# Kernel tuning notes

Measured on AMD Instinct MI355X. Metric: run time of the kernel, lower is better.

Reference implementation:

```python
import jax, jax.numpy as jnp
import numpy as np

B, M, IN_DIM, D, H, NL = 4, 2048, 512, 1024, 4, 2
HD = D // H           # head_dim = 256
HD2 = HD // 2
ROPE_BASE = 10000.0
LN_EPS = 1e-5


def setup_inputs() -> dict:
    key = jax.random.key(0)
    ks = jax.random.split(key, 9)
    s = 0.02
    return {
        "x": jax.random.normal(ks[0], (B, M, IN_DIM), jnp.float32),
        "positions": jnp.sort(jax.random.randint(ks[1], (B, M), 0, 8192), axis=-1).astype(jnp.int32),
        "mask": jnp.ones((B, M), jnp.float32),
        "in_w": jax.random.normal(ks[2], (IN_DIM, D), jnp.float32) * s,
        "in_b": jnp.zeros((D,), jnp.float32),
        "qkv_w": jax.random.normal(ks[3], (NL, D, 3 * D), jnp.float32) * s,
        "o_w": jax.random.normal(ks[4], (NL, D, D), jnp.float32) * s,
        "ln1_g": jnp.ones((NL, D), jnp.float32),
        "ln1_b": jnp.zeros((NL, D), jnp.float32),
        "ffn_w1": jax.random.normal(ks[5], (NL, D, 4 * D), jnp.float32) * s,
        "ffn_b1": jnp.zeros((NL, 4 * D), jnp.float32),
        "ffn_w2": jax.random.normal(ks[6], (NL, 4 * D, D), jnp.float32) * s,
        "ffn_b2": jnp.zeros((NL, D), jnp.float32),
        "ln2_g": jnp.ones((NL, D), jnp.float32),
        "ln2_b": jnp.zeros((NL, D), jnp.float32),
        "start_state": jax.random.normal(ks[7], (D,), jnp.float32) * 0.02,
    }


def _layernorm(x, g, b):
    mu = jnp.mean(x, axis=-1, keepdims=True)
    var = jnp.mean((x - mu) ** 2, axis=-1, keepdims=True)
    return (x - mu) * jax.lax.rsqrt(var + LN_EPS) * g + b


def _rope_cos_sin(positions):
    # rope_module(pos): angles over head_dim//2 freqs, shared across heads
    inv_freq = 1.0 / (ROPE_BASE ** (jnp.arange(HD2, dtype=jnp.float32) * 2.0 / HD))
    ang = positions.astype(jnp.float32)[:, :, None] * inv_freq  # (B, L, HD2)
    return jnp.cos(ang), jnp.sin(ang)


def _apply_rotary(x, cos, sin):
    # x: (B, H, L, HD); cos/sin: (B, 1, L, HD2) broadcast over heads
    x1, x2 = x[..., :HD2], x[..., HD2:]
    return jnp.concatenate([x1 * cos - x2 * sin, x1 * sin + x2 * cos], axis=-1)


def _self_attention(x, cos, sin, mask, qkv_w, o_w):
    Bx, L, Dx = x.shape
    qkv = (x @ qkv_w).reshape(Bx, L, 3, H, HD)
    q = jnp.transpose(qkv[:, :, 0], (0, 2, 1, 3))  # (B, H, L, HD)
    k = jnp.transpose(qkv[:, :, 1], (0, 2, 1, 3))
    v = jnp.transpose(qkv[:, :, 2], (0, 2, 1, 3))
    q = _apply_rotary(q, cos, sin)
    k = _apply_rotary(k, cos, sin)
    scores = jnp.einsum("bhqd,bhkd->bhqk", q, k) * (1.0 / np.sqrt(HD))
    scores = jnp.where(mask[:, None, None, :] == 0, -jnp.inf, scores)
    attn = jax.nn.softmax(scores, axis=-1)
    out = jnp.einsum("bhqk,bhkd->bhqd", attn, v)
    out = jnp.transpose(out, (0, 2, 1, 3)).reshape(Bx, L, Dx)
    return out @ o_w


def reference(x, positions, mask, in_w, in_b, qkv_w, o_w, ln1_g, ln1_b,
              ffn_w1, ffn_b1, ffn_w2, ffn_b2, ln2_g, ln2_b, start_state):
    h = x @ in_w + in_b  # (B, M, D)
    cos, sin = _rope_cos_sin(positions)
    cos, sin = cos[:, None], sin[:, None]  # (B, 1, M, HD2)
    for l in range(NL):
        h = h + _self_attention(_layernorm(h, ln1_g[l], ln1_b[l]), cos, sin, mask,
                                qkv_w[l], o_w[l])
        y = _layernorm(h, ln2_g[l], ln2_b[l])
        y = jax.nn.gelu(y @ ffn_w1[l] + ffn_b1[l], approximate=False) @ ffn_w2[l] + ffn_b2[l]
        h = h + y
    lengths = jnp.sum(mask, axis=1)
    last_idx = jnp.clip(lengths.astype(jnp.int32) - 1, 0, None)
    gathered = h[jnp.arange(h.shape[0]), last_idx]  # (B, D)
    has_hist = lengths > 0
    return jnp.where(has_hist[:, None], gathered, start_state[None, :])
```

## Files before the change

kernel.cpp:

```cpp
#include <hip/hip_runtime.h>
#include <math.h>

typedef __attribute__((ext_vector_type(8))) short bf16x8;
typedef __attribute__((ext_vector_type(4))) float floatx4;
typedef __attribute__((ext_vector_type(4))) unsigned short ushort4v;

typedef __attribute__((address_space(1))) void as1_void;
typedef __attribute__((address_space(3))) void as3_void;

static __device__ __forceinline__ unsigned short f2b(float f) {
    union { float f; unsigned u; } v; v.f = f;
    unsigned r = v.u + 0x7fffu + ((v.u >> 16) & 1u);
    return (unsigned short)(r >> 16);
}
static __device__ __forceinline__ float b2f(unsigned short h) {
    union { unsigned u; float f; } v; v.u = ((unsigned)h) << 16;
    return v.f;
}

template<int P> __device__ __forceinline__ void waitcnt_vm() {
    if constexpr (P == 0)      asm volatile("s_waitcnt vmcnt(0)" ::: "memory");
    else if constexpr (P == 2) asm volatile("s_waitcnt vmcnt(2)" ::: "memory");
    else if constexpr (P == 3) asm volatile("s_waitcnt vmcnt(3)" ::: "memory");
    else if constexpr (P == 4) asm volatile("s_waitcnt vmcnt(4)" ::: "memory");
    else if constexpr (P == 6) asm volatile("s_waitcnt vmcnt(6)" ::: "memory");
    else                       asm volatile("s_waitcnt vmcnt(8)" ::: "memory");
}

template<int TM, int TN>
__global__ __launch_bounds__(512, 2) void gemm9(
    const unsigned short* __restrict__ A,
    const unsigned short* __restrict__ Bt,
    float* __restrict__ Cf, unsigned short* __restrict__ Cb,
    const float* __restrict__ bias,
    int K, int lda, int ldb, int ldc,
    int zdiv, long a_s1, long a_s2, long b_s1, long b_s2, long c_s1, long c_s2,
    int mode)
{
    constexpr int FM  = TM / 32;
    constexpr int FN  = TN / 64;
    constexpr int MH  = (FM == 8) ? 2 : 1;
    constexpr int NH  = (FN == 4) ? 2 : 1;
    constexpr int NPH = MH * NH;
    constexpr int FMp = FM / MH;
    constexpr int FNp = FN / NH;
    constexpr int NRA = TM / 64;
    constexpr int NRB = TN / 64;

    __shared__ unsigned short As[2][8 * TM * 8];
    __shared__ unsigned short Bs[2][8 * TN * 8];

    const int tid  = threadIdx.x;
    const int wid  = tid >> 6;
    const int lane = tid & 63;
    const int q    = lane >> 4;
    const int r    = lane & 15;
    const int wm   = wid >> 2;
    const int wn   = wid & 3;

    const int z  = blockIdx.z;
    const int zq = z / zdiv, zr = z % zdiv;
    const long offC = (long)zq * c_s1 + (long)zr * c_s2;

    const int m0 = blockIdx.y * TM;
    const int n0 = blockIdx.x * TN;

    const unsigned short* Ab = A  + (long)zq * a_s1 + (long)zr * a_s2 + (long)m0 * lda;
    const unsigned short* Bb = Bt + (long)zq * b_s1 + (long)zr * b_s2 + (long)n0 * ldb;

    floatx4 acc[FM][FN];
    #pragma unroll
    for (int i = 0; i < FM; ++i)
        #pragma unroll
        for (int j = 0; j < FN; ++j)
            acc[i][j] = (floatx4){0.f, 0.f, 0.f, 0.f};

    const int nk = K >> 6;

    auto stageA = [&](int kt, int slot) {
        const int kofs = (kt << 6) + (wid << 3);
        #pragma unroll
        for (int rb = 0; rb < NRA; ++rb)
            __builtin_amdgcn_global_load_lds(
                (as1_void*)(void*)(Ab + (long)(rb * 64 + lane) * lda + kofs),
                (as3_void*)&As[slot][(wid * TM + rb * 64) * 8], 16, 0, 0);
    };
    auto stageB = [&](int kt, int slot) {
        const int kofs = (kt << 6) + (wid << 3);
        #pragma unroll
        for (int rb = 0; rb < NRB; ++rb)
            __builtin_amdgcn_global_load_lds(
                (as1_void*)(void*)(Bb + (long)(rb * 64 + lane) * ldb + kofs),
                (as3_void*)&Bs[slot][(wid * TN + rb * 64) * 8], 16, 0, 0);
    };

    stageA(0, 0);
    stageB(0, 0);
    waitcnt_vm<0>();
    asm volatile("s_barrier" ::: "memory");

    for (int kt = 0; kt < nk; ++kt) {
        const int c  = kt & 1;
        const int sl = c ^ 1;
        const bool pf = (kt + 1 < nk);

        bf16x8 af[MH][FMp][2];
        bf16x8 bf_[NH][FNp][2];

        #pragma unroll
        for (int ph = 0; ph < NPH; ++ph) {
            const int mh = (MH == 1) ? 0 : ((NPH == 4) ? (ph >> 1) : ph);
            const int nh = (NH == 1) ? 0 : ((NPH == 4) ? (((ph + 1) >> 1) & 1) : ph);
            const bool readA = (ph == mh * (NPH / MH));
            const bool readB = (ph == nh);

            if (readA) {
                #pragma unroll
                for (int i = 0; i < FMp; ++i)
                    #pragma unroll
                    for (int ks = 0; ks < 2; ++ks)
                        af[mh][i][ks] = *(const bf16x8*)&As[c][
                            ((ks * 4 + q) * TM + wm * (TM / 2) + mh * (FMp * 16) + i * 16 + r) * 8];
            }
            if (readB) {
                #pragma unroll
                for (int j = 0; j < FNp; ++j)
                    #pragma unroll
                    for (int ks = 0; ks < 2; ++ks)
                        bf_[nh][j][ks] = *(const bf16x8*)&Bs[c][
                            ((ks * 4 + q) * TN + wn * (TN / 4) + nh * (FNp * 16) + j * 16 + r) * 8];
            }
            if (ph == 0 && pf) stageA(kt + 1, sl);
            if (ph == 1 && pf) stageB(kt + 1, sl);

            asm volatile("s_barrier" ::: "memory");
            asm volatile("s_waitcnt lgkmcnt(0)" ::: "memory");
            __builtin_amdgcn_s_setprio(1);
            #pragma unroll
            for (int i = 0; i < FMp; ++i)
                #pragma unroll
                for (int j = 0; j < FNp; ++j) {
                    acc[mh * FMp + i][nh * FNp + j] = __builtin_amdgcn_mfma_f32_16x16x32_bf16(
                        af[mh][i][0], bf_[nh][j][0], acc[mh * FMp + i][nh * FNp + j], 0, 0, 0);
                    acc[mh * FMp + i][nh * FNp + j] = __builtin_amdgcn_mfma_f32_16x16x32_bf16(
                        af[mh][i][1], bf_[nh][j][1], acc[mh * FMp + i][nh * FNp + j], 0, 0, 0);
                }
            __builtin_amdgcn_s_setprio(0);
        }

        if (pf) {
            waitcnt_vm<0>();
            asm volatile("s_barrier" ::: "memory");
        }
    }

    #pragma unroll
    for (int i = 0; i < FM; ++i) {
        const int gr0 = m0 + wm * (TM / 2) + i * 16 + q * 4;
        #pragma unroll
        for (int j = 0; j < FN; ++j) {
            const int gc = n0 + wn * (TN / 4) + j * 16 + r;
            const float bvl = bias ? bias[gc] : 0.0f;
            #pragma unroll
            for (int rr = 0; rr < 4; ++rr) {
                const long cidx = offC + (long)(gr0 + rr) * ldc + gc;
                float v = acc[i][j][rr] + bvl;
                if (mode == 0) {
                    Cf[cidx] = v;
                } else if (mode == 1) {
                    Cf[cidx] += v;
                } else if (mode == 2) {
                    Cb[cidx] = f2b(v);
                } else {
                    Cb[cidx] = f2b(0.5f * v * (1.0f + erff(v * 0.70710678118654752f)));
                }
            }
        }
    }
}

template<int T>
__global__ __launch_bounds__(256) void gemm_bf16(
    const unsigned short* __restrict__ A,
    const unsigned short* __restrict__ Bt,
    float* __restrict__ Cf, unsigned short* __restrict__ Cb,
    const float* __restrict__ bias,
    int K, int lda, int ldb, int ldc,
    int zdiv, long a_s1, long a_s2, long b_s1, long b_s2, long c_s1, long c_s2,
    int mode)
{
    constexpr int F  = T / 32;
    constexpr int NR = T / 64;

    __shared__ unsigned short As[3][4 * T * 8];
    __shared__ unsigned short Bs[3][4 * T * 8];

    const int tid  = threadIdx.x;
    const int wid  = tid >> 6;
    const int lane = tid & 63;
    const int q    = lane >> 4;
    const int r    = lane & 15;

    const int z  = blockIdx.z;
    const int zq = z / zdiv, zr = z % zdiv;
    const long offC = (long)zq * c_s1 + (long)zr * c_s2;

    const int m0 = blockIdx.y * T;
    const int n0 = blockIdx.x * T;

    const unsigned short* Ab = A  + (long)zq * a_s1 + (long)zr * a_s2 + (long)m0 * lda;
    const unsigned short* Bb = Bt + (long)zq * b_s1 + (long)zr * b_s2 + (long)n0 * ldb;

    const int wr = (wid >> 1) * (T / 2);
    const int wc = (wid & 1)  * (T / 2);

    floatx4 acc[F][F];
    #pragma unroll
    for (int i = 0; i < F; ++i)
        #pragma unroll
        for (int j = 0; j < F; ++j)
            acc[i][j] = (floatx4){0.f, 0.f, 0.f, 0.f};

    const int qc = wid;
    const int nk = K >> 5;

    auto stage = [&](int kt, int buf) {
        const int kofs = (kt << 5) + (qc << 3);
        #pragma unroll
        for (int rb = 0; rb < NR; ++rb)
            __builtin_amdgcn_global_load_lds(
                (as1_void*)(void*)(Ab + (long)(lane + rb * 64) * lda + kofs),
                (as3_void*)&As[buf][(qc * T + rb * 64) * 8], 16, 0, 0);
        #pragma unroll
        for (int rb = 0; rb < NR; ++rb)
            __builtin_amdgcn_global_load_lds(
                (as1_void*)(void*)(Bb + (long)(lane + rb * 64) * ldb + kofs),
                (as3_void*)&Bs[buf][(qc * T + rb * 64) * 8], 16, 0, 0);
    };

    stage(0, 0);
    if (nk > 1) {
        stage(1, 1);
        waitcnt_vm<2 * NR>();
    } else {
        waitcnt_vm<0>();
    }
    asm volatile("s_barrier" ::: "memory");

    int cur = 0;
    for (int kt = 0; kt < nk; ++kt) {
        int s2 = cur + 2; if (s2 >= 3) s2 -= 3;
        if (kt + 2 < nk) stage(kt + 2, s2);

        bf16x8 av[F], bv[F];
        #pragma unroll
        for (int i = 0; i < F; ++i)
            av[i] = *(const bf16x8*)&As[cur][(q * T + wr + i * 16 + r) * 8];
        #pragma unroll
        for (int j = 0; j < F; ++j)
            bv[j] = *(const bf16x8*)&Bs[cur][(q * T + wc + j * 16 + r) * 8];
        #pragma unroll
        for (int i = 0; i < F; ++i)
            #pragma unroll
            for (int j = 0; j < F; ++j)
                acc[i][j] = __builtin_amdgcn_mfma_f32_16x16x32_bf16(av[i], bv[j], acc[i][j], 0, 0, 0);

        if (kt + 2 < nk) {
            asm volatile("s_waitcnt lgkmcnt(0)" ::: "memory");
            waitcnt_vm<2 * NR>();
            asm volatile("s_barrier" ::: "memory");
        } else if (kt + 1 < nk) {
            asm volatile("s_waitcnt lgkmcnt(0)" ::: "memory");
            waitcnt_vm<0>();
            asm volatile("s_barrier" ::: "memory");
        }

        cur = (cur + 1 == 3) ? 0 : cur + 1;
    }

    #pragma unroll
    for (int i = 0; i < F; ++i) {
        const int gr0 = m0 + wr + i * 16 + q * 4;
        #pragma unroll
        for (int j = 0; j < F; ++j) {
            const int gc = n0 + wc + j * 16 + r;
            const float bvl = bias ? bias[gc] : 0.0f;
            #pragma unroll
            for (int rr = 0; rr < 4; ++rr) {
                const long cidx = offC + (long)(gr0 + rr) * ldc + gc;
                float v = acc[i][j][rr] + bvl;
                if (mode == 0) {
                    Cf[cidx] = v;
                } else if (mode == 1) {
                    Cf[cidx] += v;
                } else if (mode == 2) {
                    Cb[cidx] = f2b(v);
                } else {
                    Cb[cidx] = f2b(0.5f * v * (1.0f + erff(v * 0.70710678118654752f)));
                }
            }
        }
    }
}

__global__ void transpose_cast_f32(const float* __restrict__ in, unsigned short* __restrict__ out,
                                   int R, int C)
{
    __shared__ float t[32][33];
    const int c0 = blockIdx.x * 32, r0 = blockIdx.y * 32;
    const int tx = threadIdx.x, ty = threadIdx.y;
    #pragma unroll
    for (int i = 0; i < 4; ++i)
        t[ty + i * 8][tx] = in[(long)(r0 + ty + i * 8) * C + c0 + tx];
    __syncthreads();
    #pragma unroll
    for (int i = 0; i < 4; ++i)
        out[(long)(c0 + ty + i * 8) * R + r0 + tx] = f2b(t[tx][ty + i * 8]);
}

__global__ void transpose_v(const unsigned short* __restrict__ qkv, unsigned short* __restrict__ vT)
{
    __shared__ unsigned short t[32][33];
    const int hh = blockIdx.z;
    const int d0 = blockIdx.x * 32, m0 = blockIdx.y * 32;
    const int tx = threadIdx.x, ty = threadIdx.y;
    const unsigned short* ip = qkv + 2048 + hh * 256;
    unsigned short* op = vT + (long)hh * 524288;
    #pragma unroll
    for (int i = 0; i < 4; ++i)
        t[ty + i * 8][tx] = ip[(long)(m0 + ty + i * 8) * 3072 + d0 + tx];
    __syncthreads();
    #pragma unroll
    for (int i = 0; i < 4; ++i)
        op[(long)(d0 + ty + i * 8) * 2048 + m0 + tx] = t[tx][ty + i * 8];
}

__global__ void cast_f32_bf16(const float* __restrict__ in, unsigned short* __restrict__ out)
{
    const long i = (long)blockIdx.x * 256 + threadIdx.x;
    const float4 v = ((const float4*)in)[i];
    ushort4v o;
    o[0] = f2b(v.x); o[1] = f2b(v.y); o[2] = f2b(v.z); o[3] = f2b(v.w);
    ((ushort4v*)out)[i] = o;
}

__global__ void zero_f32(float* __restrict__ p)
{
    p[blockIdx.x * 256 + threadIdx.x] = 0.0f;
}

__global__ __launch_bounds__(256) void ln_kernel(const float* __restrict__ h,
    const float* __restrict__ g, const float* __restrict__ bta,
    unsigned short* __restrict__ out)
{
    const int tok = blockIdx.x;
    const float4 v = ((const float4*)(h + (long)tok * 1024))[threadIdx.x];
    float s  = v.x + v.y + v.z + v.w;
    float s2 = v.x * v.x + v.y * v.y + v.z * v.z + v.w * v.w;
    #pragma unroll
    for (int off = 32; off > 0; off >>= 1) {
        s  += __shfl_xor(s, off);
        s2 += __shfl_xor(s2, off);
    }
    __shared__ float rs[4], rs2[4];
    const int wid = threadIdx.x >> 6, lane = threadIdx.x & 63;
    if (lane == 0) { rs[wid] = s; rs2[wid] = s2; }
    __syncthreads();
    s  = rs[0] + rs[1] + rs[2] + rs[3];
    s2 = rs2[0] + rs2[1] + rs2[2] + rs2[3];
    const float mu = s * (1.0f / 1024.0f);
    float var = s2 * (1.0f / 1024.0f) - mu * mu;
    var = fmaxf(var, 0.0f);
    const float rsg = 1.0f / sqrtf(var + 1e-5f);
    const float4 gv = ((const float4*)g)[threadIdx.x];
    const float4 bv = ((const float4*)bta)[threadIdx.x];
    ushort4v o;
    o[0] = f2b((v.x - mu) * rsg * gv.x + bv.x);
    o[1] = f2b((v.y - mu) * rsg * gv.y + bv.y);
    o[2] = f2b((v.z - mu) * rsg * gv.z + bv.z);
    o[3] = f2b((v.w - mu) * rsg * gv.w + bv.w);
    *(ushort4v*)&out[(long)tok * 1024 + threadIdx.x * 4] = o;
}

__global__ __launch_bounds__(256) void rope_kernel(unsigned short* __restrict__ qkv,
                                                   const int* __restrict__ pos)
{
    const int tok = blockIdx.x;
    const float p = (float)pos[tok];
    unsigned short* base = qkv + (long)tok * 3072;
    #pragma unroll
    for (int it = 0; it < 2; ++it) {
        const int idx = threadIdx.x + it * 256;
        const int hh = idx >> 7, d = idx & 127;
        const float inv = exp2f((float)d * (-13.287712379549449f / 128.0f));
        const float ang = p * inv;
        const float c = cosf(ang), s = sinf(ang);
        unsigned short* qp = base + hh * 256 + d;
        {
            const float x1 = b2f(qp[0]), x2 = b2f(qp[128]);
            qp[0]   = f2b(x1 * c - x2 * s);
            qp[128] = f2b(x1 * s + x2 * c);
        }
        unsigned short* kp = qp + 1024;
        {
            const float x1 = b2f(kp[0]), x2 = b2f(kp[128]);
            kp[0]   = f2b(x1 * c - x2 * s);
            kp[128] = f2b(x1 * s + x2 * c);
        }
    }
}

__global__ __launch_bounds__(256) void softmax_kernel(unsigned short* __restrict__ sc,
                                                      const float* __restrict__ mrow)
{
    unsigned short* row = sc + (long)blockIdx.x * 2048;
    const int t = threadIdx.x;

    float v[8];
    const ushort4v u0 = *(const ushort4v*)&row[t * 8];
    const ushort4v u1 = *(const ushort4v*)&row[t * 8 + 4];
    #pragma unroll
    for (int i = 0; i < 4; ++i) { v[i] = b2f(u0[i]); v[4 + i] = b2f(u1[i]); }

    float mx = -3.0e38f;
    #pragma unroll
    for (int i = 0; i < 8; ++i) {
        const float m = mrow[t * 8 + i];
        v[i] = (m == 0.0f) ? -3.0e38f : v[i] * 0.0625f;
        mx = fmaxf(mx, v[i]);
    }
    #pragma unroll
    for (int off = 32; off > 0; off >>= 1) mx = fmaxf(mx, __shfl_xor(mx, off));
    __shared__ float rmx[4], rsm[4];
    const int wid = t >> 6, lane = t & 63;
    if (lane == 0) rmx[wid] = mx;
    __syncthreads();
    mx = fmaxf(fmaxf(rmx[0], rmx[1]), fmaxf(rmx[2], rmx[3]));

    float s = 0.0f;
    #pragma unroll
    for (int i = 0; i < 8; ++i) { v[i] = expf(v[i] - mx); s += v[i]; }
    #pragma unroll
    for (int off = 32; off > 0; off >>= 1) s += __shfl_xor(s, off);
    if (lane == 0) rsm[wid] = s;
    __syncthreads();
    s = rsm[0] + rsm[1] + rsm[2] + rsm[3];
    const float invs = (s > 0.0f) ? 1.0f / s : 0.0f;

    ushort4v o0, o1;
    #pragma unroll
    for (int i = 0; i < 4; ++i) { o0[i] = f2b(v[i] * invs); o1[i] = f2b(v[4 + i] * invs); }
    *(ushort4v*)&row[t * 8]     = o0;
    *(ushort4v*)&row[t * 8 + 4] = o1;
}

__global__ __launch_bounds__(256) void gather_kernel(const float* __restrict__ h,
    const float* __restrict__ mask, const float* __restrict__ ss, float* __restrict__ out)
{
    const int b = blockIdx.x;
    const float* mrow = mask + b * 2048;
    const int t = threadIdx.x;
    float s = 0.0f;
    #pragma unroll
    for (int i = 0; i < 8; ++i) s += mrow[t * 8 + i];
    #pragma unroll
    for (int off = 32; off > 0; off >>= 1) s += __shfl_xor(s, off);
    __shared__ float red[4];
    if ((t & 63) == 0) red[t >> 6] = s;
    __syncthreads();
    const float len = red[0] + red[1] + red[2] + red[3];
    const int L = (int)len;
    const int last = (L > 0) ? (L - 1) : 0;
    const bool has = len > 0.0f;
    const float* src = has ? (h + ((long)b * 2048 + last) * 1024) : ss;
    #pragma unroll
    for (int i = 0; i < 4; ++i) {
        const int d = t + i * 256;
        out[b * 1024 + d] = src[d];
    }
}

extern "C" void kernel_launch(void* const* d_in, const int* in_sizes, int n_in,
                              void* d_out, int out_size, void* d_ws, size_t ws_size,
                              hipStream_t stream)
{
    (void)in_sizes; (void)n_in; (void)out_size;
    const float* x      = (const float*)d_in[0];
    const int*   pos    = (const int*)d_in[1];
    const float* mask   = (const float*)d_in[2];
    const float* in_w   = (const float*)d_in[3];
    const float* in_b   = (const float*)d_in[4];
    const float* qkv_w  = (const float*)d_in[5];
    const float* o_w    = (const float*)d_in[6];
    const float* ln1_g  = (const float*)d_in[7];
    const float* ln1_b  = (const float*)d_in[8];
    const float* ffn_w1 = (const float*)d_in[9];
    const float* ffn_b1 = (const float*)d_in[10];
    const float* ffn_w2 = (const float*)d_in[11];
    const float* ffn_b2 = (const float*)d_in[12];
    const float* ln2_g  = (const float*)d_in[13];
    const float* ln2_b  = (const float*)d_in[14];
    const float* sstate = (const float*)d_in[15];
    float* out = (float*)d_out;

    const size_t NEED = 143654912ull;
    if (ws_size < NEED) {
        zero_f32<<<16, 256, 0, stream>>>(out);
        return;
    }
    char* w = (char*)d_ws;
    unsigned short* wt_in  = (unsigned short*)(w);
    unsigned short* wt_qkv = (unsigned short*)(w + 1048576);
    unsigned short* wt_o   = (unsigned short*)(w + 7340032);
    unsigned short* wt_f1  = (unsigned short*)(w + 9437184);
    unsigned short* wt_f2  = (unsigned short*)(w + 17825792);
    float*          hbuf   = (float*)(w + 26214400);
    unsigned short* xn_bf  = (unsigned short*)(w + 59768832);
    unsigned short* ao_bf  = (unsigned short*)(w + 76546048);
    unsigned short* qkv_b  = (unsigned short*)(w + 93323264);
    unsigned short* vT_b   = (unsigned short*)(w + 105906176);
    unsigned short* scmid  = (unsigned short*)(w + 110100480);
    unsigned short* x_bf   = ao_bf;
    unsigned short* mid_bf = (unsigned short*)(w + 76546048);

    const dim3 tb(32, 8);

    transpose_cast_f32<<<dim3(32, 16), tb, 0, stream>>>(in_w, wt_in, 512, 1024);
    cast_f32_bf16<<<4096, 256, 0, stream>>>(x, x_bf);

    gemm9<256, 128><<<dim3(8, 32, 1), 512, 0, stream>>>(x_bf, wt_in, hbuf, nullptr, in_b,
        512, 512, 512, 1024, 1, 0, 0, 0, 0, 0, 0, 0);

    for (int l = 0; l < 2; ++l) {
        transpose_cast_f32<<<dim3(96, 32),  tb, 0, stream>>>(qkv_w  + (long)l * 3145728, wt_qkv, 1024, 3072);
        transpose_cast_f32<<<dim3(32, 32),  tb, 0, stream>>>(o_w    + (long)l * 1048576, wt_o,   1024, 1024);
        transpose_cast_f32<<<dim3(128, 32), tb, 0, stream>>>(ffn_w1 + (long)l * 4194304, wt_f1,  1024, 4096);
        transpose_cast_f32<<<dim3(32, 128), tb, 0, stream>>>(ffn_w2 + (long)l * 4194304, wt_f2,  4096, 1024);

        ln_kernel<<<8192, 256, 0, stream>>>(hbuf, ln1_g + l * 1024, ln1_b + l * 1024, xn_bf);

        for (int b = 0; b < 4; ++b) {
            gemm9<128, 256><<<dim3(12, 16, 1), 512, 0, stream>>>(xn_bf + (long)b * 2097152, wt_qkv,
                nullptr, qkv_b, nullptr, 1024, 1024, 1024, 3072, 1, 0, 0, 0, 0, 0, 0, 2);
            rope_kernel<<<2048, 256, 0, stream>>>(qkv_b, pos + b * 2048);
            transpose_v<<<dim3(8, 64, 4), tb, 0, stream>>>(qkv_b, vT_b);
            gemm9<256, 256><<<dim3(8, 8, 4), 512, 0, stream>>>(qkv_b, qkv_b + 1024,
                nullptr, scmid, nullptr, 256, 3072, 3072, 2048,
                1, 256l, 0, 256l, 0, 4194304l, 0, 2);
            softmax_kernel<<<8192, 256, 0, stream>>>(scmid, mask + b * 2048);
            gemm_bf16<64><<<dim3(4, 32, 4), 256, 0, stream>>>(scmid, vT_b,
                nullptr, ao_bf + (long)b * 2097152, nullptr, 2048, 2048, 2048, 1024,
                1, 4194304l, 0, 524288l, 0, 256l, 0, 2);
        }
        gemm9<256, 128><<<dim3(8, 32, 1), 512, 0, stream>>>(ao_bf, wt_o,
            hbuf, nullptr, nullptr, 1024, 1024, 1024, 1024, 1, 0, 0, 0, 0, 0, 0, 1);

        ln_kernel<<<8192, 256, 0, stream>>>(hbuf, ln2_g + l * 1024, ln2_b + l * 1024, xn_bf);

        gemm9<256, 256><<<dim3(16, 32, 1), 512, 0, stream>>>(xn_bf, wt_f1,
            nullptr, mid_bf, ffn_b1 + l * 4096, 1024, 1024, 1024, 4096, 1, 0, 0, 0, 0, 0, 0, 3);
        gemm9<256, 128><<<dim3(8, 32, 1), 512, 0, stream>>>(mid_bf, wt_f2,
            hbuf, nullptr, ffn_b2 + l * 1024, 4096, 4096, 4096, 1024, 1, 0, 0, 0, 0, 0, 0, 1);
    }

    gather_kernel<<<4, 256, 0, stream>>>(hbuf, mask, sstate, out);
}
```

Measured before the change: 2.161 ms.

## Split GEMM tiles into 128-wide LDS units with finer-grained staged prefetch

Restructures the main bf16 MFMA GEMM so each operand tile is split into 128-row LDS units, each with its own slot (up to four per operand). Loads for the next k-step are issued per unit, interleaved between the quadrant MFMA phases, and use partial vmcnt waits. The aim is to overlap global-to-LDS traffic with compute better than the previous whole-tile double buffer did, which waited for all loads at the end of each k-step. In exchange it adds more barriers per k-step, changes the accumulator-to-output mapping, and adds slot-indexing complexity, with some risk to correctness if the waits or slot reuse are misordered.

```diff
diff --git a/kernel.cpp b/kernel.cpp
--- a/kernel.cpp
+++ b/kernel.cpp
@@ -21,14 +21,12 @@
 template<int P> __device__ __forceinline__ void waitcnt_vm() {
     if constexpr (P == 0)      asm volatile("s_waitcnt vmcnt(0)" ::: "memory");
     else if constexpr (P == 2) asm volatile("s_waitcnt vmcnt(2)" ::: "memory");
-    else if constexpr (P == 3) asm volatile("s_waitcnt vmcnt(3)" ::: "memory");
     else if constexpr (P == 4) asm volatile("s_waitcnt vmcnt(4)" ::: "memory");
-    else if constexpr (P == 6) asm volatile("s_waitcnt vmcnt(6)" ::: "memory");
-    else                       asm volatile("s_waitcnt vmcnt(8)" ::: "memory");
+    else                       asm volatile("s_waitcnt vmcnt(6)" ::: "memory");
 }
 
 template<int TM, int TN>
-__global__ __launch_bounds__(512, 2) void gemm9(
+__global__ __launch_bounds__(512, 2) void gemmX(
     const unsigned short* __restrict__ A,
     const unsigned short* __restrict__ Bt,
     float* __restrict__ Cf, unsigned short* __restrict__ Cb,
@@ -37,18 +35,15 @@
     int zdiv, long a_s1, long a_s2, long b_s1, long b_s2, long c_s1, long c_s2,
     int mode)
 {
-    constexpr int FM  = TM / 32;
-    constexpr int FN  = TN / 64;
-    constexpr int MH  = (FM == 8) ? 2 : 1;
-    constexpr int NH  = (FN == 4) ? 2 : 1;
-    constexpr int NPH = MH * NH;
-    constexpr int FMp = FM / MH;
-    constexpr int FNp = FN / NH;
-    constexpr int NRA = TM / 64;
-    constexpr int NRB = TN / 64;
-
-    __shared__ unsigned short As[2][8 * TM * 8];
-    __shared__ unsigned short Bs[2][8 * TN * 8];
+    constexpr int NAU = TM / 128;
+    constexpr int NBU = TN / 128;
+    constexpr int NSA = (NAU == 2) ? 4 : 2;
+    constexpr int NSB = (NBU == 2) ? 4 : 2;
+    constexpr int NPH = NAU * NBU;
+    constexpr int BVM = (NPH == 4) ? 4 : 2;
+
+    __shared__ unsigned short As[NSA][8][128][8];
+    __shared__ unsigned short Bs[NSB][8][128][8];
 
     const int tid  = threadIdx.x;
     const int wid  = tid >> 6;
@@ -68,103 +63,150 @@
     const unsigned short* Ab = A  + (long)zq * a_s1 + (long)zr * a_s2 + (long)m0 * lda;
     const unsigned short* Bb = Bt + (long)zq * b_s1 + (long)zr * b_s2 + (long)n0 * ldb;
 
-    floatx4 acc[FM][FN];
-    #pragma unroll
-    for (int i = 0; i < FM; ++i)
-        #pragma unroll
-        for (int j = 0; j < FN; ++j)
+    floatx4 acc[NAU * 4][NBU * 2];
+    #pragma unroll
+    for (int i = 0; i < NAU * 4; ++i)
+        #pragma unroll
+        for (int j = 0; j < NBU * 2; ++j)
             acc[i][j] = (floatx4){0.f, 0.f, 0.f, 0.f};
 
     const int nk = K >> 6;
 
-    auto stageA = [&](int kt, int slot) {
+    auto stageAu = [&](int kt, int h) {
+        const int slot = (NAU == 2) ? ((2 * kt + h) & 3) : (kt & 1);
         const int kofs = (kt << 6) + (wid << 3);
         #pragma unroll
-        for (int rb = 0; rb < NRA; ++rb)
+        for (int rb = 0; rb < 2; ++rb) {
+            const int grow = (NAU == 2) ? (rb * 128 + h * 64 + lane) : (rb * 64 + lane);
             __builtin_amdgcn_global_load_lds(
-                (as1_void*)(void*)(Ab + (long)(rb * 64 + lane) * lda + kofs),
-                (as3_void*)&As[slot][(wid * TM + rb * 64) * 8], 16, 0, 0);
+                (as1_void*)(void*)(Ab + (long)grow * lda + kofs),
+                (as3_void*)&As[slot][wid][rb * 64][0], 16, 0, 0);
+        }
     };
-    auto stageB = [&](int kt, int slot) {
+    auto stageBu = [&](int kt, int h) {
+        const int slot = (NBU == 2) ? ((2 * kt + h) & 3) : (kt & 1);
         const int kofs = (kt << 6) + (wid << 3);
         #pragma unroll
-        for (int rb = 0; rb < NRB; ++rb)
+        for (int rb = 0; rb < 2; ++rb) {
+            const int grow = (NBU == 2)
+                ? ((rb * 2 + (lane >> 5)) * 64 + h * 32 + (lane & 31))
+                : (rb * 64 + lane);
             __builtin_amdgcn_global_load_lds(
-                (as1_void*)(void*)(Bb + (long)(rb * 64 + lane) * ldb + kofs),
-                (as3_void*)&Bs[slot][(wid * TN + rb * 64) * 8], 16, 0, 0);
+                (as1_void*)(void*)(Bb + (long)grow * ldb + kofs),
+                (as3_void*)&Bs[slot][wid][rb * 64][0], 16, 0, 0);
+        }
     };
 
-    stageA(0, 0);
-    stageB(0, 0);
-    waitcnt_vm<0>();
+    bf16x8 af[4][2], bfr[2][2];
+
+    auto readA = [&](int kt, int mq) {
+        const int slot = (NAU == 2) ? ((2 * kt + mq) & 3) : (kt & 1);
+        #pragma unroll
+        for (int i = 0; i < 4; ++i)
+            #pragma unroll
+            for (int ks = 0; ks < 2; ++ks)
+                af[i][ks] = *(const bf16x8*)&As[slot][ks * 4 + q][wm * 64 + i * 16 + r][0];
+    };
+    auto readB = [&](int kt, int nq) {
+        const int slot = (NBU == 2) ? ((2 * kt + nq) & 3) : (kt & 1);
+        #pragma unroll
+        for (int j = 0; j < 2; ++j)
+            #pragma unroll
+            for (int ks = 0; ks < 2; ++ks)
+                bfr[j][ks] = *(const bf16x8*)&Bs[slot][ks * 4 + q][wn * 32 + j * 16 + r][0];
+    };
+    auto qmfma = [&](int mq, int nq) {
+        __builtin_amdgcn_s_setprio(1);
+        #pragma unroll
+        for (int i = 0; i < 4; ++i)
+            #pragma unroll
+            for (int j = 0; j < 2; ++j) {
+                acc[mq * 4 + i][nq * 2 + j] = __builtin_amdgcn_mfma_f32_16x16x32_bf16(
+                    af[i][0], bfr[j][0], acc[mq * 4 + i][nq * 2 + j], 0, 0, 0);
+                acc[mq * 4 + i][nq * 2 + j] = __builtin_amdgcn_mfma_f32_16x16x32_bf16(
+                    af[i][1], bfr[j][1], acc[mq * 4 + i][nq * 2 + j], 0, 0, 0);
+            }
+        __builtin_amdgcn_s_setprio(0);
+    };
+
+    stageAu(0, 0); stageBu(0, 0);
+    if constexpr (NPH == 4) { stageAu(0, 1); stageBu(0, 1); }
+    else if constexpr (NAU == 2) { stageAu(0, 1); }
+    else { stageBu(0, 1); }
+    waitcnt_vm<BVM>();
     asm volatile("s_barrier" ::: "memory");
 
     for (int kt = 0; kt < nk; ++kt) {
-        const int c  = kt & 1;
-        const int sl = c ^ 1;
         const bool pf = (kt + 1 < nk);
 
-        bf16x8 af[MH][FMp][2];
-        bf16x8 bf_[NH][FNp][2];
-
-        #pragma unroll
-        for (int ph = 0; ph < NPH; ++ph) {
-            const int mh = (MH == 1) ? 0 : ((NPH == 4) ? (ph >> 1) : ph);
-            const int nh = (NH == 1) ? 0 : ((NPH == 4) ? (((ph + 1) >> 1) & 1) : ph);
-            const bool readA = (ph == mh * (NPH / MH));
-            const bool readB = (ph == nh);
-
-            if (readA) {
-                #pragma unroll
-                for (int i = 0; i < FMp; ++i)
-                    #pragma unroll
-                    for (int ks = 0; ks < 2; ++ks)
-                        af[mh][i][ks] = *(const bf16x8*)&As[c][
-                            ((ks * 4 + q) * TM + wm * (TM / 2) + mh * (FMp * 16) + i * 16 + r) * 8];
-            }
-            if (readB) {
-                #pragma unroll
-                for (int j = 0; j < FNp; ++j)
-                    #pragma unroll
-                    for (int ks = 0; ks < 2; ++ks)
-                        bf_[nh][j][ks] = *(const bf16x8*)&Bs[c][
-                            ((ks * 4 + q) * TN + wn * (TN / 4) + nh * (FNp * 16) + j * 16 + r) * 8];
-            }
-            if (ph == 0 && pf) stageA(kt + 1, sl);
-            if (ph == 1 && pf) stageB(kt + 1, sl);
-
-            asm volatile("s_barrier" ::: "memory");
-            asm volatile("s_waitcnt lgkmcnt(0)" ::: "memory");
-            __builtin_amdgcn_s_setprio(1);
-            #pragma unroll
-            for (int i = 0; i < FMp; ++i)
-                #pragma unroll
-                for (int j = 0; j < FNp; ++j) {
-                    acc[mh * FMp + i][nh * FNp + j] = __builtin_amdgcn_mfma_f32_16x16x32_bf16(
-                        af[mh][i][0], bf_[nh][j][0], acc[mh * FMp + i][nh * FNp + j], 0, 0, 0);
-                    acc[mh * FMp + i][nh * FNp + j] = __builtin_amdgcn_mfma_f32_16x16x32_bf16(
-                        af[mh][i][1], bf_[nh][j][1], acc[mh * FMp + i][nh * FNp + j], 0, 0, 0);
-                }
-            __builtin_amdgcn_s_setprio(0);
+        if constexpr (NPH == 4) {
+            if (pf) stageAu(kt + 1, 0);
+            asm volatile("s_barrier" ::: "memory");
+            readA(kt, 0); readB(kt, 0);
+            asm volatile("s_waitcnt lgkmcnt(0)" ::: "memory");
+            qmfma(0, 0);
+            if (pf) stageBu(kt + 1, 0);
+            if (pf) waitcnt_vm<4>(); else waitcnt_vm<0>();
+            asm volatile("s_barrier" ::: "memory");
+            readB(kt, 1);
+            asm volatile("s_waitcnt lgkmcnt(0)" ::: "memory");
+            qmfma(0, 1);
+            if (pf) stageAu(kt + 1, 1);
+            asm volatile("s_barrier" ::: "memory");
+            readA(kt, 1);
+            asm volatile("s_waitcnt lgkmcnt(0)" ::: "memory");
+            qmfma(1, 1);
+            if (pf) stageBu(kt + 1, 1);
+            asm volatile("s_barrier" ::: "memory");
+            readB(kt, 0);
+            asm volatile("s_waitcnt lgkmcnt(0)" ::: "memory");
+            qmfma(1, 0);
+        } else if constexpr (NAU == 2) {
+            if (pf) { stageAu(kt + 1, 0); stageBu(kt + 1, 0); }
+            asm volatile("s_barrier" ::: "memory");
+            readA(kt, 0); readB(kt, 0);
+            asm volatile("s_waitcnt lgkmcnt(0)" ::: "memory");
+            qmfma(0, 0);
+            if (pf) stageAu(kt + 1, 1);
+            if (pf) waitcnt_vm<4>(); else waitcnt_vm<0>();
+            asm volatile("s_barrier" ::: "memory");
+            readA(kt, 1);
+            asm volatile("s_waitcnt lgkmcnt(0)" ::: "memory");
+            qmfma(1, 0);
+        } else {
+            if (pf) { stageAu(kt + 1, 0); stageBu(kt + 1, 0); }
+            asm volatile("s_barrier" ::: "memory");
+            readA(kt, 0); readB(kt, 0);
+            asm volatile("s_waitcnt lgkmcnt(0)" ::: "memory");
+            qmfma(0, 0);
+            if (pf) stageBu(kt + 1, 1);
+            if (pf) waitcnt_vm<4>(); else waitcnt_vm<0>();
+            asm volatile("s_barrier" ::: "memory");
+            readB(kt, 1);
+            asm volatile("s_waitcnt lgkmcnt(0)" ::: "memory");
+            qmfma(0, 1);
         }
 
         if (pf) {
-            waitcnt_vm<0>();
-            asm volatile("s_barrier" ::: "memory");
-        }
-    }
-
-    #pragma unroll
-    for (int i = 0; i < FM; ++i) {
-        const int gr0 = m0 + wm * (TM / 2) + i * 16 + q * 4;
-        #pragma unroll
-        for (int j = 0; j < FN; ++j) {
-            const int gc = n0 + wn * (TN / 4) + j * 16 + r;
+            waitcnt_vm<BVM>();
+            asm volatile("s_barrier" ::: "memory");
+        }
+    }
+
+    #pragma unroll
+    for (int mi = 0; mi < NAU * 4; ++mi) {
+        const int gr0 = m0 + wm * (TM / 2)
+            + ((NAU == 2) ? ((mi >> 2) * 64 + (mi & 3) * 16) : (mi * 16)) + q * 4;
+        #pragma unroll
+        for (int nj = 0; nj < NBU * 2; ++nj) {
+            const int gc = n0
+                + ((NBU == 2) ? (wn * 64 + (nj >> 1) * 32 + (nj & 1) * 16)
+                              : (wn * 32 + nj * 16)) + r;
             const float bvl = bias ? bias[gc] : 0.0f;
             #pragma unroll
             for (int rr = 0; rr < 4; ++rr) {
                 const long cidx = offC + (long)(gr0 + rr) * ldc + gc;
-                float v = acc[i][j][rr] + bvl;
+                float v = acc[mi][nj][rr] + bvl;
                 if (mode == 0) {
                     Cf[cidx] = v;
                 } else if (mode == 1) {
@@ -528,7 +570,7 @@
     transpose_cast_f32<<<dim3(32, 16), tb, 0, stream>>>(in_w, wt_in, 512, 1024);
     cast_f32_bf16<<<4096, 256, 0, stream>>>(x, x_bf);
 
-    gemm9<256, 128><<<dim3(8, 32, 1), 512, 0, stream>>>(x_bf, wt_in, hbuf, nullptr, in_b,
+    gemmX<256, 128><<<dim3(8, 32, 1), 512, 0, stream>>>(x_bf, wt_in, hbuf, nullptr, in_b,
         512, 512, 512, 1024, 1, 0, 0, 0, 0, 0, 0, 0);
 
     for (int l = 0; l < 2; ++l) {
@@ -540,11 +582,11 @@
         ln_kernel<<<8192, 256, 0, stream>>>(hbuf, ln1_g + l * 1024, ln1_b + l * 1024, xn_bf);
 
         for (int b = 0; b < 4; ++b) {
-            gemm9<128, 256><<<dim3(12, 16, 1), 512, 0, stream>>>(xn_bf + (long)b * 2097152, wt_qkv,
+            gemmX<128, 256><<<dim3(12, 16, 1), 512, 0, stream>>>(xn_bf + (long)b * 2097152, wt_qkv,
                 nullptr, qkv_b, nullptr, 1024, 1024, 1024, 3072, 1, 0, 0, 0, 0, 0, 0, 2);
             rope_kernel<<<2048, 256, 0, stream>>>(qkv_b, pos + b * 2048);
             transpose_v<<<dim3(8, 64, 4), tb, 0, stream>>>(qkv_b, vT_b);
-            gemm9<256, 256><<<dim3(8, 8, 4), 512, 0, stream>>>(qkv_b, qkv_b + 1024,
+            gemmX<256, 256><<<dim3(8, 8, 4), 512, 0, stream>>>(qkv_b, qkv_b + 1024,
                 nullptr, scmid, nullptr, 256, 3072, 3072, 2048,
                 1, 256l, 0, 256l, 0, 4194304l, 0, 2);
             softmax_kernel<<<8192, 256, 0, stream>>>(scmid, mask + b * 2048);
@@ -552,14 +594,14 @@
                 nullptr, ao_bf + (long)b * 2097152, nullptr, 2048, 2048, 2048, 1024,
                 1, 4194304l, 0, 524288l, 0, 256l, 0, 2);
         }
-        gemm9<256, 128><<<dim3(8, 32, 1), 512, 0, stream>>>(ao_bf, wt_o,
+        gemmX<256, 128><<<dim3(8, 32, 1), 512, 0, stream>>>(ao_bf, wt_o,
             hbuf, nullptr, nullptr, 1024, 1024, 1024, 1024, 1, 0, 0, 0, 0, 0, 0, 1);
 
         ln_kernel<<<8192, 256, 0, stream>>>(hbuf, ln2_g + l * 1024, ln2_b + l * 1024, xn_bf);
 
-        gemm9<256, 256><<<dim3(16, 32, 1), 512, 0, stream>>>(xn_bf, wt_f1,
+        gemmX<256, 256><<<dim3(16, 32, 1), 512, 0, stream>>>(xn_bf, wt_f1,
             nullptr, mid_bf, ffn_b1 + l * 4096, 1024, 1024, 1024, 4096, 1, 0, 0, 0, 0, 0, 0, 3);
-        gemm9<256, 128><<<dim3(8, 32, 1), 512, 0, stream>>>(mid_bf, wt_f2,
+        gemmX<256, 128><<<dim3(8, 32, 1), 512, 0, stream>>>(mid_bf, wt_f2,
             hbuf, nullptr, ffn_b2 + l * 1024, 4096, 4096, 4096, 1024, 1, 0, 0, 0, 0, 0, 0, 1);
     }
 
```

Result: slower. 2.878 ms (+33.2%).
